# Performance work log

Measured on AMD Instinct MI355X. Metric: run time of the kernel, lower is better.

## Reference

```python
import jax, jax.numpy as jnp
import numpy as np

N_WIRES = 8
DIM = 1 << N_WIRES  # 256

# Precompute CNOT permutations (torchquantum convention: wire 0 = MSB)
_idx = np.arange(DIM)
_CNOT_PERMS = []
for _c in range(N_WIRES):
    _t = (_c + 1) % N_WIRES
    _cbit = (_idx >> (N_WIRES - 1 - _c)) & 1
    _CNOT_PERMS.append(np.where(_cbit == 1, _idx ^ (1 << (N_WIRES - 1 - _t)), _idx))
# PauliZ signs per wire: [DIM, N_WIRES]
_ZSIGNS = np.stack([1.0 - 2.0 * ((_idx >> (N_WIRES - 1 - w)) & 1) for w in range(N_WIRES)], axis=1).astype(np.float32)


def _quantum_heads(x, theta):
    """x: [B,S,H,8] angles; theta: [8]. Returns PauliZ expectations [B,S,H,8].

    Simulates per (token,head) an 8-qubit circuit: RX(x_i+theta_i) on wire i
    (encoder RX followed by trainable RX on same wire = one RX with summed angle),
    then CNOT ring 0->1..6->7, 7->0, then MeasureAll PauliZ.
    """
    B, S, H, _ = x.shape
    N = B * S * H
    ang = x.reshape(N, N_WIRES) + theta  # [N,8]
    state = jnp.zeros((N, DIM), dtype=jnp.complex64).at[:, 0].set(1.0)
    half = ang * 0.5
    c_all = jnp.cos(half)
    s_all = jnp.sin(half)
    for w in range(N_WIRES):
        A = 1 << w
        Bdim = 1 << (N_WIRES - 1 - w)
        s = state.reshape(N, A, 2, Bdim)
        a0, a1 = s[:, :, 0, :], s[:, :, 1, :]
        c = c_all[:, w][:, None, None].astype(jnp.complex64)
        isn = (1j * s_all[:, w][:, None, None]).astype(jnp.complex64)
        n0 = c * a0 - isn * a1
        n1 = -isn * a0 + c * a1
        state = jnp.stack([n0, n1], axis=2).reshape(N, DIM)
    for perm in _CNOT_PERMS:
        state = state[:, perm]
    probs = state.real ** 2 + state.imag ** 2  # [N,256]
    exp = probs @ jnp.asarray(_ZSIGNS)  # [N,8]
    return exp.reshape(B, S, H, N_WIRES)


def _mha(proj, W_combine, num_heads):
    # proj: [B,S,E]; q = k = v = proj (identical deterministic projections)
    B, S, E = proj.shape
    d_k = E // num_heads
    qkv = proj.reshape(B, S, num_heads, d_k).transpose(0, 2, 1, 3)  # [B,H,S,dk]
    scores = jnp.einsum('bhqd,bhkd->bhqk', qkv, qkv) / jnp.sqrt(jnp.float32(d_k))
    attn = jax.nn.softmax(scores, axis=-1)
    out = jnp.einsum('bhqk,bhkd->bhqd', attn, qkv)
    out = out.transpose(0, 2, 1, 3).reshape(B, S, E)
    return out @ W_combine.T


def setup_inputs() -> dict:
    key = jax.random.key(0)
    k1, k2, k3 = jax.random.split(key, 3)
    B, S, H = 8, 1024, 8
    E = H * N_WIRES  # 64
    x = jax.random.normal(k1, (B, S, E), dtype=jnp.float32)
    theta = jax.random.normal(k2, (N_WIRES,), dtype=jnp.float32)
    W_combine = jax.random.normal(k3, (E, E), dtype=jnp.float32) * (1.0 / np.sqrt(E))
    return {'x': x, 'theta': theta, 'W_combine': W_combine}


def reference(x, theta, W_combine):
    B, S, E = x.shape
    H = E // N_WIRES
    proj = _quantum_heads(x.reshape(B, S, H, N_WIRES), theta).reshape(B, S, E)
    return _mha(proj, W_combine, H)
```

## Files before the change

kernel.cpp:

```cpp
#include <hip/hip_runtime.h>

typedef _Float16 half4v __attribute__((ext_vector_type(4)));
typedef __fp16 fp16x2 __attribute__((ext_vector_type(2)));
typedef float float4v __attribute__((ext_vector_type(4)));

#define S_ 1024
#define H_ 8
#define B_ 8
#define BH 64
#define NROW 8192
#define E_ 64
#define VST 1032

static __device__ inline half4v pack4(float a, float b, float c, float d) {
    union { fp16x2 f2[2]; half4v h4; } u;
    u.f2[0] = __builtin_amdgcn_cvt_pkrtz(a, b);
    u.f2[1] = __builtin_amdgcn_cvt_pkrtz(c, d);
    return u.h4;
}

__global__ __launch_bounds__(256, 4) void attn_kernel(
        const float* __restrict__ x, const float* __restrict__ theta,
        _Float16* __restrict__ attnH) {
    __shared__ _Float16 kF[64 * 128];
    __shared__ _Float16 vT[9 * VST];
    int bh = blockIdx.x;
    int b = bh >> 3, h = bh & 7;
    int tid = threadIdx.x;

    float th[8];
#pragma unroll
    for (int i = 0; i < 8; ++i) th[i] = theta[i];

    {
        const half4v one = {(_Float16)1.f, (_Float16)1.f, (_Float16)1.f, (_Float16)1.f};
        *(half4v*)&vT[8 * VST + tid * 4] = one;
    }

    for (int s = tid; s < S_; s += 256) {
        const float4* xp = (const float4*)(x + (((size_t)(b << 10) + s) << 6) + (h << 3));
        float4 x0 = xp[0];
        float4 x1 = xp[1];
        float c0 = __cosf(x0.x + th[0]);
        float c1 = __cosf(x0.y + th[1]);
        float c2 = __cosf(x0.z + th[2]);
        float c3 = __cosf(x0.w + th[3]);
        float c4 = __cosf(x1.x + th[4]);
        float c5 = __cosf(x1.y + th[5]);
        float c6 = __cosf(x1.z + th[6]);
        float c7 = __cosf(x1.w + th[7]);
        float e1 = c0 * c1;
        float e2 = e1 * c2;
        float e3 = e2 * c3;
        float e4 = e3 * c4;
        float e5 = e4 * c5;
        float e6 = e5 * c6;
        float e7 = e6 * c7;
        float e0 = ((c1 * c2) * (c3 * c4)) * ((c5 * c6) * c7);
        half4v lo = pack4(e0, e1, e2, e3);
        half4v hi = pack4(e4, e5, e6, e7);
        int kt = s >> 4, c = s & 15;
        *(half4v*)&kF[kt * 128 + c * 4]      = lo;
        *(half4v*)&kF[kt * 128 + 64 + c * 4] = hi;
        vT[0 * VST + s] = lo[0]; vT[1 * VST + s] = lo[1];
        vT[2 * VST + s] = lo[2]; vT[3 * VST + s] = lo[3];
        vT[4 * VST + s] = hi[0]; vT[5 * VST + s] = hi[1];
        vT[6 * VST + s] = hi[2]; vT[7 * VST + s] = hi[3];
    }
    __syncthreads();

    int lane = tid & 63;
    int wv   = tid >> 6;
    int col  = lane & 15;
    int quad = lane >> 4;
    int q0   = blockIdx.y * 64 + wv * 16;

    bool lo2 = (quad < 2);

    int kbase = (lane & 31) * 4;
    int vcol = (col < 9) ? col : (col - 8);
    int vbase = vcol * VST + quad * 4;

    half4v qf = {(_Float16)0.f, (_Float16)0.f, (_Float16)0.f, (_Float16)0.f};
    if (lo2) qf = *(const half4v*)&kF[kbase + (q0 >> 4) * 128];
    qf *= (_Float16)0.51012921f;

    const float4v zc = {0.f, 0.f, 0.f, 0.f};
    float4v o0 = zc, o1 = zc, o2 = zc, o3 = zc;

#pragma unroll
    for (int kt = 0; kt < 16; ++kt) {
        half4v k0 = *(const half4v*)&kF[kbase + (kt +  0) * 128];
        half4v k1 = *(const half4v*)&kF[kbase + (kt + 16) * 128];
        half4v k2 = *(const half4v*)&kF[kbase + (kt + 32) * 128];
        half4v k3 = *(const half4v*)&kF[kbase + (kt + 48) * 128];
        half4v v0 = *(const half4v*)&vT[vbase + (kt +  0) * 16];
        half4v v1 = *(const half4v*)&vT[vbase + (kt + 16) * 16];
        half4v v2 = *(const half4v*)&vT[vbase + (kt + 32) * 16];
        half4v v3 = *(const half4v*)&vT[vbase + (kt + 48) * 16];
        float4v s0 = __builtin_amdgcn_mfma_f32_16x16x16f16(k0, qf, zc, 0, 0, 0);
        float4v s1 = __builtin_amdgcn_mfma_f32_16x16x16f16(k1, qf, zc, 0, 0, 0);
        float4v s2 = __builtin_amdgcn_mfma_f32_16x16x16f16(k2, qf, zc, 0, 0, 0);
        float4v s3 = __builtin_amdgcn_mfma_f32_16x16x16f16(k3, qf, zc, 0, 0, 0);
        half4v p0 = pack4(__builtin_amdgcn_exp2f(s0[0]), __builtin_amdgcn_exp2f(s0[1]),
                          __builtin_amdgcn_exp2f(s0[2]), __builtin_amdgcn_exp2f(s0[3]));
        half4v p1 = pack4(__builtin_amdgcn_exp2f(s1[0]), __builtin_amdgcn_exp2f(s1[1]),
                          __builtin_amdgcn_exp2f(s1[2]), __builtin_amdgcn_exp2f(s1[3]));
        half4v p2 = pack4(__builtin_amdgcn_exp2f(s2[0]), __builtin_amdgcn_exp2f(s2[1]),
                          __builtin_amdgcn_exp2f(s2[2]), __builtin_amdgcn_exp2f(s2[3]));
        half4v p3 = pack4(__builtin_amdgcn_exp2f(s3[0]), __builtin_amdgcn_exp2f(s3[1]),
                          __builtin_amdgcn_exp2f(s3[2]), __builtin_amdgcn_exp2f(s3[3]));
        o0 = __builtin_amdgcn_mfma_f32_16x16x16f16(v0, p0, o0, 0, 0, 0);
        o1 = __builtin_amdgcn_mfma_f32_16x16x16f16(v1, p1, o1, 0, 0, 0);
        o2 = __builtin_amdgcn_mfma_f32_16x16x16f16(v2, p2, o2, 0, 0, 0);
        o3 = __builtin_amdgcn_mfma_f32_16x16x16f16(v3, p3, o3, 0, 0, 0);
    }

    float4v oacc;
#pragma unroll
    for (int r = 0; r < 4; ++r) oacc[r] = (o0[r] + o1[r]) + (o2[r] + o3[r]);

    float l = __shfl(oacc[0], 32 | col, 64);
    if (lo2) {
        float inv = __builtin_amdgcn_rcpf(l);
        half4v ov = pack4(oacc[0] * inv, oacc[1] * inv, oacc[2] * inv, oacc[3] * inv);
        *(half4v*)(attnH + (((size_t)(b << 10) + q0 + col) << 6) + (h << 3) + quad * 4) = ov;
    }
}

__global__ __launch_bounds__(256) void combine_kernel(
        const _Float16* __restrict__ AH, const float* __restrict__ W,
        float* __restrict__ out) {
    __shared__ _Float16 a2[64 * 68];
    __shared__ _Float16 wt[64 * 68];
    int r0 = blockIdx.x * 64;
    int tid = threadIdx.x;

    for (int idx = tid; idx < E_ * E_; idx += 256) {
        int e = idx >> 6, k = idx & 63;
        wt[k * 68 + e] = (_Float16)W[idx];
    }
#pragma unroll
    for (int j = 0; j < 4; ++j) {
        int off = tid * 16 + j * 4;
        int row = off >> 6, k = off & 63;
        *(half4v*)&a2[row * 68 + k] = *(const half4v*)&AH[(size_t)r0 * E_ + off];
    }
    __syncthreads();

    int lane = tid & 63;
    int wv   = tid >> 6;
    int col  = lane & 15;
    int quad = lane >> 4;

    half4v wf[4][4];
#pragma unroll
    for (int t = 0; t < 4; ++t)
#pragma unroll
        for (int e = 0; e < 4; ++e) {
            int kb = (t * 16 + quad * 4) * 68 + e * 16 + col;
            half4v w_ = {wt[kb], wt[kb + 68], wt[kb + 136], wt[kb + 204]};
            wf[t][e] = w_;
        }

    float4v acc[4] = {{0,0,0,0},{0,0,0,0},{0,0,0,0},{0,0,0,0}};
#pragma unroll
    for (int t = 0; t < 4; ++t) {
        half4v af = *(const half4v*)&a2[(wv * 16 + col) * 68 + t * 16 + quad * 4];
#pragma unroll
        for (int e = 0; e < 4; ++e)
            acc[e] = __builtin_amdgcn_mfma_f32_16x16x16f16(af, wf[t][e], acc[e], 0, 0, 0);
    }

#pragma unroll
    for (int e = 0; e < 4; ++e)
#pragma unroll
        for (int r = 0; r < 4; ++r)
            out[(size_t)(r0 + wv * 16 + quad * 4 + r) * E_ + e * 16 + col] = acc[e][r];
}

extern "C" void kernel_launch(void* const* d_in, const int* in_sizes, int n_in,
                              void* d_out, int out_size, void* d_ws, size_t ws_size,
                              hipStream_t stream) {
    const float* x     = (const float*)d_in[0];
    const float* theta = (const float*)d_in[1];
    const float* W     = (const float*)d_in[2];
    float* out = (float*)d_out;

    _Float16* attnH = (_Float16*)d_ws;

    attn_kernel<<<dim3(BH, S_ / 64), 256, 0, stream>>>(x, theta, attnH);
    combine_kernel<<<NROW / 64, 256, 0, stream>>>(attnH, W, out);
}
```

Before: 73.02 us.

## Split projection into separate kernel, stream K/V from global instead of LDS

Moves the cosine-product projection out of the attention kernel into a new proj_kernel that writes K and an MFMA-ready V layout (with the ones column for the softmax denominator) to workspace. The attention kernel then reads K and V straight from global memory (served by cache) and no longer uses shared memory or a block barrier. Previously each of the 16 query blocks per head recomputed the full projection. This removes that redundant work and LDS pressure, at the cost of an extra launch and global or L2 traffic in the inner loop.

```diff
diff --git a/kernel.cpp b/kernel.cpp
--- a/kernel.cpp
+++ b/kernel.cpp
@@ -10,7 +10,6 @@
 #define BH 64
 #define NROW 8192
 #define E_ 64
-#define VST 1032
 
 static __device__ inline half4v pack4(float a, float b, float c, float d) {
     union { fp16x2 f2[2]; half4v h4; } u;
@@ -19,70 +18,71 @@
     return u.h4;
 }
 
+__global__ __launch_bounds__(256) void proj_kernel(
+        const float* __restrict__ x, const float* __restrict__ theta,
+        _Float16* __restrict__ kG, _Float16* __restrict__ vG) {
+    int bh = blockIdx.x >> 2;
+    int s  = ((blockIdx.x & 3) << 8) + threadIdx.x;
+    int b = bh >> 3, h = bh & 7;
+
+    const float4* xp = (const float4*)(x + (((size_t)(b << 10) + s) << 6) + (h << 3));
+    float4 x0 = xp[0];
+    float4 x1 = xp[1];
+    float c0 = __cosf(x0.x + theta[0]);
+    float c1 = __cosf(x0.y + theta[1]);
+    float c2 = __cosf(x0.z + theta[2]);
+    float c3 = __cosf(x0.w + theta[3]);
+    float c4 = __cosf(x1.x + theta[4]);
+    float c5 = __cosf(x1.y + theta[5]);
+    float c6 = __cosf(x1.z + theta[6]);
+    float c7 = __cosf(x1.w + theta[7]);
+    float e1 = c0 * c1;
+    float e2 = e1 * c2;
+    float e3 = e2 * c3;
+    float e4 = e3 * c4;
+    float e5 = e4 * c5;
+    float e6 = e5 * c6;
+    float e7 = e6 * c7;
+    float e0 = ((c1 * c2) * (c3 * c4)) * ((c5 * c6) * c7);
+    half4v lo = pack4(e0, e1, e2, e3);
+    half4v hi = pack4(e4, e5, e6, e7);
+
+    int kt = s >> 4, c = s & 15;
+    _Float16* kgb = kG + (size_t)bh * 8192;
+    _Float16* vgb = vG + (size_t)bh * 16384;
+    *(half4v*)&kgb[kt * 128 + c * 4]      = lo;
+    *(half4v*)&kgb[kt * 128 + 64 + c * 4] = hi;
+
+    _Float16 arr[9] = {lo[0], lo[1], lo[2], lo[3], hi[0], hi[1], hi[2], hi[3],
+                       (_Float16)1.0f};
+    int quad = c >> 2, j = c & 3;
+    int base = kt * 256 + (quad << 6) + j;
+#pragma unroll
+    for (int col = 0; col < 16; ++col) {
+        vgb[base + col * 4] = arr[(col < 9) ? col : (col - 8)];
+    }
+}
+
 __global__ __launch_bounds__(256, 4) void attn_kernel(
-        const float* __restrict__ x, const float* __restrict__ theta,
+        const _Float16* __restrict__ kG, const _Float16* __restrict__ vG,
         _Float16* __restrict__ attnH) {
-    __shared__ _Float16 kF[64 * 128];
-    __shared__ _Float16 vT[9 * VST];
     int bh = blockIdx.x;
     int b = bh >> 3, h = bh & 7;
     int tid = threadIdx.x;
-
-    float th[8];
-#pragma unroll
-    for (int i = 0; i < 8; ++i) th[i] = theta[i];
-
-    {
-        const half4v one = {(_Float16)1.f, (_Float16)1.f, (_Float16)1.f, (_Float16)1.f};
-        *(half4v*)&vT[8 * VST + tid * 4] = one;
-    }
-
-    for (int s = tid; s < S_; s += 256) {
-        const float4* xp = (const float4*)(x + (((size_t)(b << 10) + s) << 6) + (h << 3));
-        float4 x0 = xp[0];
-        float4 x1 = xp[1];
-        float c0 = __cosf(x0.x + th[0]);
-        float c1 = __cosf(x0.y + th[1]);
-        float c2 = __cosf(x0.z + th[2]);
-        float c3 = __cosf(x0.w + th[3]);
-        float c4 = __cosf(x1.x + th[4]);
-        float c5 = __cosf(x1.y + th[5]);
-        float c6 = __cosf(x1.z + th[6]);
-        float c7 = __cosf(x1.w + th[7]);
-        float e1 = c0 * c1;
-        float e2 = e1 * c2;
-        float e3 = e2 * c3;
-        float e4 = e3 * c4;
-        float e5 = e4 * c5;
-        float e6 = e5 * c6;
-        float e7 = e6 * c7;
-        float e0 = ((c1 * c2) * (c3 * c4)) * ((c5 * c6) * c7);
-        half4v lo = pack4(e0, e1, e2, e3);
-        half4v hi = pack4(e4, e5, e6, e7);
-        int kt = s >> 4, c = s & 15;
-        *(half4v*)&kF[kt * 128 + c * 4]      = lo;
-        *(half4v*)&kF[kt * 128 + 64 + c * 4] = hi;
-        vT[0 * VST + s] = lo[0]; vT[1 * VST + s] = lo[1];
-        vT[2 * VST + s] = lo[2]; vT[3 * VST + s] = lo[3];
-        vT[4 * VST + s] = hi[0]; vT[5 * VST + s] = hi[1];
-        vT[6 * VST + s] = hi[2]; vT[7 * VST + s] = hi[3];
-    }
-    __syncthreads();
-
     int lane = tid & 63;
     int wv   = tid >> 6;
     int col  = lane & 15;
     int quad = lane >> 4;
     int q0   = blockIdx.y * 64 + wv * 16;
-
     bool lo2 = (quad < 2);
 
-    int kbase = (lane & 31) * 4;
-    int vcol = (col < 9) ? col : (col - 8);
-    int vbase = vcol * VST + quad * 4;
+    const _Float16* kgb = kG + (size_t)bh * 8192;
+    const _Float16* vgb = vG + (size_t)bh * 16384;
+    int kaddr = (lane & 31) * 4;
+    int vaddr = lane * 4;
 
     half4v qf = {(_Float16)0.f, (_Float16)0.f, (_Float16)0.f, (_Float16)0.f};
-    if (lo2) qf = *(const half4v*)&kF[kbase + (q0 >> 4) * 128];
+    if (lo2) qf = *(const half4v*)&kgb[kaddr + (q0 >> 4) * 128];
     qf *= (_Float16)0.51012921f;
 
     const float4v zc = {0.f, 0.f, 0.f, 0.f};
@@ -90,14 +90,14 @@
 
 #pragma unroll
     for (int kt = 0; kt < 16; ++kt) {
-        half4v k0 = *(const half4v*)&kF[kbase + (kt +  0) * 128];
-        half4v k1 = *(const half4v*)&kF[kbase + (kt + 16) * 128];
-        half4v k2 = *(const half4v*)&kF[kbase + (kt + 32) * 128];
-        half4v k3 = *(const half4v*)&kF[kbase + (kt + 48) * 128];
-        half4v v0 = *(const half4v*)&vT[vbase + (kt +  0) * 16];
-        half4v v1 = *(const half4v*)&vT[vbase + (kt + 16) * 16];
-        half4v v2 = *(const half4v*)&vT[vbase + (kt + 32) * 16];
-        half4v v3 = *(const half4v*)&vT[vbase + (kt + 48) * 16];
+        half4v k0 = *(const half4v*)&kgb[kaddr + (kt +  0) * 128];
+        half4v k1 = *(const half4v*)&kgb[kaddr + (kt + 16) * 128];
+        half4v k2 = *(const half4v*)&kgb[kaddr + (kt + 32) * 128];
+        half4v k3 = *(const half4v*)&kgb[kaddr + (kt + 48) * 128];
+        half4v v0 = *(const half4v*)&vgb[vaddr + (kt +  0) * 256];
+        half4v v1 = *(const half4v*)&vgb[vaddr + (kt + 16) * 256];
+        half4v v2 = *(const half4v*)&vgb[vaddr + (kt + 32) * 256];
+        half4v v3 = *(const half4v*)&vgb[vaddr + (kt + 48) * 256];
         float4v s0 = __builtin_amdgcn_mfma_f32_16x16x16f16(k0, qf, zc, 0, 0, 0);
         float4v s1 = __builtin_amdgcn_mfma_f32_16x16x16f16(k1, qf, zc, 0, 0, 0);
         float4v s2 = __builtin_amdgcn_mfma_f32_16x16x16f16(k2, qf, zc, 0, 0, 0);
@@ -188,7 +188,10 @@
     float* out = (float*)d_out;
 
     _Float16* attnH = (_Float16*)d_ws;
+    _Float16* kG    = (_Float16*)((char*)d_ws + (1 << 20));
+    _Float16* vG    = (_Float16*)((char*)d_ws + (2 << 20));
 
-    attn_kernel<<<dim3(BH, S_ / 64), 256, 0, stream>>>(x, theta, attnH);
+    proj_kernel<<<BH * 4, 256, 0, stream>>>(x, theta, kG, vG);
+    attn_kernel<<<dim3(BH, S_ / 64), 256, 0, stream>>>(kG, vG, attnH);
     combine_kernel<<<NROW / 64, 256, 0, stream>>>(attnH, W, out);
 }
```

Result: slower. 80.64 us (+10.4%).

## Split attention keys across two blocks and merge partial sums in combine

Applied to the files above, without the earlier changes.

Adds a grid z-dimension that splits the 1024 keys into two halves. Each block builds only its half of K/V in shared memory, plus a separate small Q tile, and writes unnormalized fp32 partial outputs and row sums to workspace. The combine kernel adds the two partials and normalizes before the output projection. This halves the per-block prologue and shared memory, which allows higher occupancy (launch bounds raised to 8) and twice as many blocks. The cost is extra fp32 workspace traffic and a second read in the combine stage.

```diff
diff --git a/kernel.cpp b/kernel.cpp
--- a/kernel.cpp
+++ b/kernel.cpp
@@ -10,7 +10,9 @@
 #define BH 64
 #define NROW 8192
 #define E_ 64
-#define VST 1032
+#define VST2 520
+#define PSTR 12
+#define KHOFF (64 * 1024 * PSTR)
 
 static __device__ inline half4v pack4(float a, float b, float c, float d) {
     union { fp16x2 f2[2]; half4v h4; } u;
@@ -19,12 +21,15 @@
     return u.h4;
 }
 
-__global__ __launch_bounds__(256, 4) void attn_kernel(
+__global__ __launch_bounds__(256, 8) void attn_kernel(
         const float* __restrict__ x, const float* __restrict__ theta,
-        _Float16* __restrict__ attnH) {
-    __shared__ _Float16 kF[64 * 128];
-    __shared__ _Float16 vT[9 * VST];
+        float* __restrict__ part) {
+    __shared__ _Float16 kF[32 * 128];
+    __shared__ _Float16 qF[4 * 128];
+    __shared__ _Float16 vT[9 * VST2];
     int bh = blockIdx.x;
+    int qt = blockIdx.y;
+    int kh = blockIdx.z;
     int b = bh >> 3, h = bh & 7;
     int tid = threadIdx.x;
 
@@ -32,13 +37,11 @@
 #pragma unroll
     for (int i = 0; i < 8; ++i) th[i] = theta[i];
 
-    {
-        const half4v one = {(_Float16)1.f, (_Float16)1.f, (_Float16)1.f, (_Float16)1.f};
-        *(half4v*)&vT[8 * VST + tid * 4] = one;
-    }
-
-    for (int s = tid; s < S_; s += 256) {
-        const float4* xp = (const float4*)(x + (((size_t)(b << 10) + s) << 6) + (h << 3));
+#pragma unroll
+    for (int i = 0; i < 2; ++i) {
+        int sl = tid + i * 256;
+        int sg = (kh << 9) + sl;
+        const float4* xp = (const float4*)(x + (((size_t)(b << 10) + sg) << 6) + (h << 3));
         float4 x0 = xp[0];
         float4 x1 = xp[1];
         float c0 = __cosf(x0.x + th[0]);
@@ -59,13 +62,39 @@
         float e0 = ((c1 * c2) * (c3 * c4)) * ((c5 * c6) * c7);
         half4v lo = pack4(e0, e1, e2, e3);
         half4v hi = pack4(e4, e5, e6, e7);
-        int kt = s >> 4, c = s & 15;
+        int kt = sl >> 4, c = sl & 15;
         *(half4v*)&kF[kt * 128 + c * 4]      = lo;
         *(half4v*)&kF[kt * 128 + 64 + c * 4] = hi;
-        vT[0 * VST + s] = lo[0]; vT[1 * VST + s] = lo[1];
-        vT[2 * VST + s] = lo[2]; vT[3 * VST + s] = lo[3];
-        vT[4 * VST + s] = hi[0]; vT[5 * VST + s] = hi[1];
-        vT[6 * VST + s] = hi[2]; vT[7 * VST + s] = hi[3];
+        vT[0 * VST2 + sl] = lo[0]; vT[1 * VST2 + sl] = lo[1];
+        vT[2 * VST2 + sl] = lo[2]; vT[3 * VST2 + sl] = lo[3];
+        vT[4 * VST2 + sl] = hi[0]; vT[5 * VST2 + sl] = hi[1];
+        vT[6 * VST2 + sl] = hi[2]; vT[7 * VST2 + sl] = hi[3];
+        vT[8 * VST2 + sl] = (_Float16)1.0f;
+    }
+    if (tid < 64) {
+        int sg = (qt << 6) + tid;
+        const float4* xp = (const float4*)(x + (((size_t)(b << 10) + sg) << 6) + (h << 3));
+        float4 x0 = xp[0];
+        float4 x1 = xp[1];
+        float c0 = __cosf(x0.x + th[0]);
+        float c1 = __cosf(x0.y + th[1]);
+        float c2 = __cosf(x0.z + th[2]);
+        float c3 = __cosf(x0.w + th[3]);
+        float c4 = __cosf(x1.x + th[4]);
+        float c5 = __cosf(x1.y + th[5]);
+        float c6 = __cosf(x1.z + th[6]);
+        float c7 = __cosf(x1.w + th[7]);
+        float e1 = c0 * c1;
+        float e2 = e1 * c2;
+        float e3 = e2 * c3;
+        float e4 = e3 * c4;
+        float e5 = e4 * c5;
+        float e6 = e5 * c6;
+        float e7 = e6 * c7;
+        float e0 = ((c1 * c2) * (c3 * c4)) * ((c5 * c6) * c7);
+        int kt = tid >> 4, c = tid & 15;
+        *(half4v*)&qF[kt * 128 + c * 4]      = pack4(e0, e1, e2, e3);
+        *(half4v*)&qF[kt * 128 + 64 + c * 4] = pack4(e4, e5, e6, e7);
     }
     __syncthreads();
 
@@ -73,63 +102,49 @@
     int wv   = tid >> 6;
     int col  = lane & 15;
     int quad = lane >> 4;
-    int q0   = blockIdx.y * 64 + wv * 16;
-
     bool lo2 = (quad < 2);
 
     int kbase = (lane & 31) * 4;
-    int vcol = (col < 9) ? col : (col - 8);
-    int vbase = vcol * VST + quad * 4;
+    int vcol  = (col < 9) ? col : (col - 8);
+    int vbase = vcol * VST2 + quad * 4;
 
     half4v qf = {(_Float16)0.f, (_Float16)0.f, (_Float16)0.f, (_Float16)0.f};
-    if (lo2) qf = *(const half4v*)&kF[kbase + (q0 >> 4) * 128];
+    if (lo2) qf = *(const half4v*)&qF[kbase + wv * 128];
     qf *= (_Float16)0.51012921f;
 
     const float4v zc = {0.f, 0.f, 0.f, 0.f};
-    float4v o0 = zc, o1 = zc, o2 = zc, o3 = zc;
-
-#pragma unroll
+    float4v o0 = zc, o1 = zc;
+
+#pragma unroll 4
     for (int kt = 0; kt < 16; ++kt) {
-        half4v k0 = *(const half4v*)&kF[kbase + (kt +  0) * 128];
+        half4v k0 = *(const half4v*)&kF[kbase + kt * 128];
         half4v k1 = *(const half4v*)&kF[kbase + (kt + 16) * 128];
-        half4v k2 = *(const half4v*)&kF[kbase + (kt + 32) * 128];
-        half4v k3 = *(const half4v*)&kF[kbase + (kt + 48) * 128];
-        half4v v0 = *(const half4v*)&vT[vbase + (kt +  0) * 16];
+        half4v v0 = *(const half4v*)&vT[vbase + kt * 16];
         half4v v1 = *(const half4v*)&vT[vbase + (kt + 16) * 16];
-        half4v v2 = *(const half4v*)&vT[vbase + (kt + 32) * 16];
-        half4v v3 = *(const half4v*)&vT[vbase + (kt + 48) * 16];
         float4v s0 = __builtin_amdgcn_mfma_f32_16x16x16f16(k0, qf, zc, 0, 0, 0);
         float4v s1 = __builtin_amdgcn_mfma_f32_16x16x16f16(k1, qf, zc, 0, 0, 0);
-        float4v s2 = __builtin_amdgcn_mfma_f32_16x16x16f16(k2, qf, zc, 0, 0, 0);
-        float4v s3 = __builtin_amdgcn_mfma_f32_16x16x16f16(k3, qf, zc, 0, 0, 0);
         half4v p0 = pack4(__builtin_amdgcn_exp2f(s0[0]), __builtin_amdgcn_exp2f(s0[1]),
                           __builtin_amdgcn_exp2f(s0[2]), __builtin_amdgcn_exp2f(s0[3]));
         half4v p1 = pack4(__builtin_amdgcn_exp2f(s1[0]), __builtin_amdgcn_exp2f(s1[1]),
                           __builtin_amdgcn_exp2f(s1[2]), __builtin_amdgcn_exp2f(s1[3]));
-        half4v p2 = pack4(__builtin_amdgcn_exp2f(s2[0]), __builtin_amdgcn_exp2f(s2[1]),
-                          __builtin_amdgcn_exp2f(s2[2]), __builtin_amdgcn_exp2f(s2[3]));
-        half4v p3 = pack4(__builtin_amdgcn_exp2f(s3[0]), __builtin_amdgcn_exp2f(s3[1]),
-                          __builtin_amdgcn_exp2f(s3[2]), __builtin_amdgcn_exp2f(s3[3]));
         o0 = __builtin_amdgcn_mfma_f32_16x16x16f16(v0, p0, o0, 0, 0, 0);
         o1 = __builtin_amdgcn_mfma_f32_16x16x16f16(v1, p1, o1, 0, 0, 0);
-        o2 = __builtin_amdgcn_mfma_f32_16x16x16f16(v2, p2, o2, 0, 0, 0);
-        o3 = __builtin_amdgcn_mfma_f32_16x16x16f16(v3, p3, o3, 0, 0, 0);
     }
 
     float4v oacc;
 #pragma unroll
-    for (int r = 0; r < 4; ++r) oacc[r] = (o0[r] + o1[r]) + (o2[r] + o3[r]);
+    for (int r = 0; r < 4; ++r) oacc[r] = o0[r] + o1[r];
 
     float l = __shfl(oacc[0], 32 | col, 64);
-    if (lo2) {
-        float inv = __builtin_amdgcn_rcpf(l);
-        half4v ov = pack4(oacc[0] * inv, oacc[1] * inv, oacc[2] * inv, oacc[3] * inv);
-        *(half4v*)(attnH + (((size_t)(b << 10) + q0 + col) << 6) + (h << 3) + quad * 4) = ov;
-    }
+    int q = (qt << 6) + (wv << 4) + col;
+    float* pp = part + ((size_t)((kh << 6) + bh) * 1024 + q) * PSTR;
+    if (lo2)
+        *(float4*)(pp + quad * 4) = make_float4(oacc[0], oacc[1], oacc[2], oacc[3]);
+    if (quad == 0) pp[8] = l;
 }
 
 __global__ __launch_bounds__(256) void combine_kernel(
-        const _Float16* __restrict__ AH, const float* __restrict__ W,
+        const float* __restrict__ part, const float* __restrict__ W,
         float* __restrict__ out) {
     __shared__ _Float16 a2[64 * 68];
     __shared__ _Float16 wt[64 * 68];
@@ -141,10 +156,23 @@
         wt[k * 68 + e] = (_Float16)W[idx];
     }
 #pragma unroll
-    for (int j = 0; j < 4; ++j) {
-        int off = tid * 16 + j * 4;
-        int row = off >> 6, k = off & 63;
-        *(half4v*)&a2[row * 68 + k] = *(const half4v*)&AH[(size_t)r0 * E_ + off];
+    for (int j = 0; j < 2; ++j) {
+        int cell = tid * 2 + j;
+        int lr = cell >> 3, h = cell & 7;
+        int r = r0 + lr;
+        int b = r >> 10, s = r & 1023;
+        size_t base = ((size_t)((b << 3) + h) * 1024 + s) * PSTR;
+        const float* p0 = part + base;
+        const float* p1 = part + KHOFF + base;
+        float4 a0 = *(const float4*)p0;
+        float4 b0 = *(const float4*)(p0 + 4);
+        float4 a1 = *(const float4*)p1;
+        float4 b1 = *(const float4*)(p1 + 4);
+        float inv = 1.0f / (p0[8] + p1[8]);
+        *(half4v*)&a2[lr * 68 + h * 8]     = pack4((a0.x + a1.x) * inv, (a0.y + a1.y) * inv,
+                                                   (a0.z + a1.z) * inv, (a0.w + a1.w) * inv);
+        *(half4v*)&a2[lr * 68 + h * 8 + 4] = pack4((b0.x + b1.x) * inv, (b0.y + b1.y) * inv,
+                                                   (b0.z + b1.z) * inv, (b0.w + b1.w) * inv);
     }
     __syncthreads();
 
@@ -187,8 +215,8 @@
     const float* W     = (const float*)d_in[2];
     float* out = (float*)d_out;
 
-    _Float16* attnH = (_Float16*)d_ws;
-
-    attn_kernel<<<dim3(BH, S_ / 64), 256, 0, stream>>>(x, theta, attnH);
-    combine_kernel<<<NROW / 64, 256, 0, stream>>>(attnH, W, out);
-}
+    float* part = (float*)d_ws;
+
+    attn_kernel<<<dim3(BH, S_ / 64, 2), 256, 0, stream>>>(x, theta, part);
+    combine_kernel<<<NROW / 64, 256, 0, stream>>>(part, W, out);
+}
```

Result: slower. 75.19 us (+3.0%).
